# Optimization experiments

Hardware: AMD Instinct MI355X
Metric: run time of the kernel (lower is better)

Reference implementation:

```python
import jax, jax.numpy as jnp
import numpy as np

B, N, IN_DIM, HID = 64, 1024, 128, 32


def _xavier(key, shape):
    # xavier_uniform_ on torch Linear weight [out, in]; we store [in, out]
    fan_in, fan_out = shape[0], shape[1]
    limit = float(np.sqrt(6.0 / (fan_in + fan_out)))
    return jax.random.uniform(key, shape, jnp.float32, -limit, limit)


def setup_inputs() -> dict:
    key = jax.random.key(0)
    ks = jax.random.split(key, 8)
    x = jax.random.normal(ks[0], (B, N, IN_DIM), jnp.float32)
    adj = jax.random.uniform(ks[1], (B, N, N), jnp.float32)  # dense adjacency
    W1 = _xavier(ks[2], (IN_DIM, HID))
    W2 = _xavier(ks[3], (HID, HID))
    W3 = _xavier(ks[4], (HID, HID))
    W4 = _xavier(ks[5], (HID, HID))
    b1 = jnp.zeros((HID,), jnp.float32)
    b2 = jnp.zeros((HID,), jnp.float32)
    b3 = jnp.zeros((HID,), jnp.float32)
    b4 = jnp.zeros((HID,), jnp.float32)
    a1 = jnp.float32(0.25)  # PReLU default init
    a2 = jnp.float32(0.25)
    a3 = jnp.float32(0.25)
    a4 = jnp.float32(0.25)
    return {"x": x, "adj": adj, "W1": W1, "W2": W2, "W3": W3, "W4": W4,
            "b1": b1, "b2": b2, "b3": b3, "b4": b4,
            "a1": a1, "a2": a2, "a3": a3, "a4": a4}


def _gcn_layer(x, adj, W, b, a):
    h = jnp.einsum('bnf,fo->bno', x, W)      # linear, no bias
    h = jnp.matmul(adj, h) + b               # aggregation + bias
    return jnp.where(h >= 0, h, a * h)       # PReLU


def reference(x, adj, W1, W2, W3, W4, b1, b2, b3, b4, a1, a2, a3, a4):
    h1 = _gcn_layer(x, adj, W1, b1, a1)
    h2 = _gcn_layer(h1, adj, W2, b2, a2)
    h3 = _gcn_layer(h2, adj, W3, b3, a3)
    h4 = _gcn_layer(h3, adj, W4, b4, a4)
    # sum-pool nodes per layer, concat along feature dim -> [B, 4*HID]
    return jnp.concatenate([h1.sum(axis=1), h2.sum(axis=1),
                            h3.sum(axis=1), h4.sum(axis=1)], axis=1)
```

## Files before the change

### kernel.cpp

```cpp
#include <hip/hip_runtime.h>
#include <hip/hip_bf16.h>

#define B_   64
#define N_   1024
#define IND_ 128
#define HID_ 32

typedef __attribute__((ext_vector_type(8))) short short8;
typedef __attribute__((ext_vector_type(4))) float f32x4;
typedef unsigned short u16;

static __device__ __forceinline__ u16 f2bf(float f) {
    union { __hip_bfloat16 h; u16 s; } u;
    u.h = __float2bfloat16(f);
    return u.s;
}
static __device__ __forceinline__ short8 cvt8(f32x4 v0, f32x4 v1) {
    union { short8 s; __hip_bfloat162 h[4]; } u;
    u.h[0] = __float22bfloat162_rn(float2{v0[0], v0[1]});
    u.h[1] = __float22bfloat162_rn(float2{v0[2], v0[3]});
    u.h[2] = __float22bfloat162_rn(float2{v1[0], v1[1]});
    u.h[3] = __float22bfloat162_rn(float2{v1[2], v1[3]});
    return u.s;
}

__global__ __launch_bounds__(256) void convert_kernel(
    const float* __restrict__ adjf, u16* __restrict__ adjb)
{
    const size_t total = (size_t)B_ * N_ * N_ / 8;
    const size_t stride = (size_t)gridDim.x * 256;
    for (size_t i = (size_t)blockIdx.x * 256 + threadIdx.x; i < total; i += stride) {
        const f32x4* src = (const f32x4*)adjf + i * 2;
        f32x4 v0 = __builtin_nontemporal_load(src);
        f32x4 v1 = __builtin_nontemporal_load(src + 1);
        ((short8*)adjb)[i] = cvt8(v0, v1);
    }
}

template<int F>
__global__ __launch_bounds__(256) void linear_kernel(
    const float* __restrict__ in,
    const float* __restrict__ W,
    u16* __restrict__ outT)
{
    __shared__ float sW[F][HID_];
    const int tid = threadIdx.x;
    for (int e = tid; e < F * HID_; e += 256) sW[e / HID_][e % HID_] = W[e];
    __syncthreads();

    const int b = blockIdx.x >> 2;
    const int n = ((blockIdx.x & 3) << 8) + tid;
    const f32x4* row4 = (const f32x4*)(in + ((size_t)b * N_ + n) * F);

    float acc[HID_];
#pragma unroll
    for (int o = 0; o < HID_; ++o) acc[o] = 0.f;

#pragma unroll 4
    for (int f4 = 0; f4 < F / 4; ++f4) {
        f32x4 xv = row4[f4];
#pragma unroll
        for (int j = 0; j < 4; ++j) {
#pragma unroll
            for (int o = 0; o < HID_; ++o) acc[o] += xv[j] * sW[f4 * 4 + j][o];
        }
    }
    u16* op = outT + (size_t)b * HID_ * N_ + n;
#pragma unroll
    for (int o = 0; o < HID_; ++o) op[o * N_] = f2bf(acc[o]);
}

template<int MODE, int FUSE>
__global__ __launch_bounds__(256) void agg_kernel(
    const float* __restrict__ adjf,
    const u16*  __restrict__ adjb_in,
    const u16*  __restrict__ hlinT_in,
    u16*        __restrict__ hlinT_out,
    const float* __restrict__ Wnext,
    float*      __restrict__ h,
    float*      __restrict__ partial,
    const float* __restrict__ bias,
    const float* __restrict__ alpha_p)
{
    union Smem {
        u16 sB[HID_][512 + 8];
        struct { float h_s[64][33]; float sW2[HID_][HID_]; } ep;
    };
    __shared__ Smem sm;
    __shared__ float pool[4][HID_];

    const int tid = threadIdx.x;
    const int b = blockIdx.y;
    const int wid = tid >> 6, lane = tid & 63;
    const int r16 = lane & 15, g = lane >> 4;
    const int koff = g * 8;
    const int rowbase = blockIdx.x * 64 + wid * 16;
    const int row0 = rowbase + r16;
    const size_t adj_b = (size_t)b * N_ * N_;
    const u16* srcB = hlinT_in + (size_t)b * HID_ * N_;

    const u16*  pa = adjb_in ? adjb_in + adj_b + (size_t)row0 * N_ + koff : nullptr;
    const float* pf = adjf   ? adjf    + adj_b + (size_t)row0 * N_ + koff : nullptr;

    f32x4 acc[2] = {};

    for (int c = 0; c < 2; ++c) {
        if (c) __syncthreads();
        for (int i = tid; i < 2048; i += 256) {
            const int row = i >> 6;
            const int kv = (i & 63) << 3;
            *(short8*)&sm.sB[row][kv] =
                *(const short8*)(srcB + (size_t)row * N_ + (c << 9) + kv);
        }
        __syncthreads();

#pragma unroll 8
        for (int kk = 0; kk < 512; kk += 32) {
            const int k0 = (c << 9) + kk;
            short8 a0;
            if (MODE == 0) {
                a0 = *(const short8*)(pa + k0);
            } else {
                f32x4 v0 = __builtin_nontemporal_load((const f32x4*)(pf + k0));
                f32x4 v1 = __builtin_nontemporal_load((const f32x4*)(pf + k0) + 1);
                a0 = cvt8(v0, v1);
            }
            short8 b0 = *(const short8*)&sm.sB[r16][kk + koff];
            short8 b1 = *(const short8*)&sm.sB[16 + r16][kk + koff];
            acc[0] = __builtin_amdgcn_mfma_f32_16x16x32_bf16(a0, b0, acc[0], 0, 0, 0);
            acc[1] = __builtin_amdgcn_mfma_f32_16x16x32_bf16(a0, b1, acc[1], 0, 0, 0);
        }
    }

    const float alpha = *alpha_p;
    float v[2][4];
    float ps[2];
#pragma unroll
    for (int ct = 0; ct < 2; ++ct) {
        const float bv = bias[ct * 16 + r16];
        ps[ct] = 0.f;
#pragma unroll
        for (int r = 0; r < 4; ++r) {
            float x = acc[ct][r] + bv;
            x = (x >= 0.f) ? x : alpha * x;
            v[ct][r] = x;
            ps[ct] += x;
        }
    }

    __syncthreads();

#pragma unroll
    for (int ct = 0; ct < 2; ++ct) {
        const int col = ct * 16 + r16;
        float p = ps[ct];
        p += __shfl_xor(p, 16, 64);
        p += __shfl_xor(p, 32, 64);
        if (lane < 16) pool[wid][col] = p;
        if (FUSE) {
#pragma unroll
            for (int r = 0; r < 4; ++r)
                sm.ep.h_s[wid * 16 + g * 4 + r][col] = v[ct][r];
        }
        if (MODE == 2) {
#pragma unroll
            for (int r = 0; r < 4; ++r) {
                const int row = rowbase + g * 4 + r;
                h[((size_t)b * N_ + row) * HID_ + col] = v[ct][r];
            }
        }
    }
    if (FUSE) {
        for (int e = tid; e < HID_ * HID_; e += 256)
            ((float*)sm.ep.sW2)[e] = Wnext[e];
    }
    __syncthreads();

    if (tid < HID_) {
        float s = pool[0][tid] + pool[1][tid] + pool[2][tid] + pool[3][tid];
        partial[((size_t)b * 16 + blockIdx.x) * HID_ + tid] = s;
    }

    if (FUSE) {
        const int r_local = tid >> 2;
        const int obase = (tid & 3) * 8;
        float acc2[8];
#pragma unroll
        for (int o = 0; o < 8; ++o) acc2[o] = 0.f;
#pragma unroll 4
        for (int k = 0; k < HID_; ++k) {
            const float hv = sm.ep.h_s[r_local][k];
#pragma unroll
            for (int o = 0; o < 8; ++o) acc2[o] += hv * sm.ep.sW2[k][obase + o];
        }
        const int n = blockIdx.x * 64 + r_local;
        u16* op = hlinT_out + (size_t)b * HID_ * N_ + n;
#pragma unroll
        for (int o = 0; o < 8; ++o) op[(size_t)(obase + o) * N_] = f2bf(acc2[o]);
    }
}

__global__ __launch_bounds__(256) void finalize_kernel(
    const float* __restrict__ partial,
    float* __restrict__ out)
{
    const int i = blockIdx.x * 256 + threadIdx.x;
    if (i >= B_ * 4 * HID_) return;
    const int b = i >> 7;
    const int rem = i & 127;
    const int l = rem >> 5;
    const int o = rem & 31;
    const float* p = partial + (((size_t)l * B_ + b) * 16) * HID_ + o;
    float s = 0.f;
#pragma unroll
    for (int t = 0; t < 16; ++t) s += p[t * HID_];
    out[i] = s;
}

extern "C" void kernel_launch(void* const* d_in, const int* in_sizes, int n_in,
                              void* d_out, int out_size, void* d_ws, size_t ws_size,
                              hipStream_t stream) {
    const float* x   = (const float*)d_in[0];
    const float* adj = (const float*)d_in[1];
    const float* W[4]  = {(const float*)d_in[2], (const float*)d_in[3],
                          (const float*)d_in[4], (const float*)d_in[5]};
    const float* bi[4] = {(const float*)d_in[6], (const float*)d_in[7],
                          (const float*)d_in[8], (const float*)d_in[9]};
    const float* al[4] = {(const float*)d_in[10], (const float*)d_in[11],
                          (const float*)d_in[12], (const float*)d_in[13]};
    float* out = (float*)d_out;

    const size_t adjb_bytes = (size_t)B_ * N_ * N_ * 2;
    const size_t hlin_bytes = (size_t)B_ * HID_ * N_ * 2;
    const size_t h_bytes    = (size_t)B_ * N_ * HID_ * 4;
    const size_t part_bytes = (size_t)4 * B_ * 16 * HID_ * 4;
    const bool full = ws_size >= adjb_bytes + 2 * hlin_bytes + part_bytes;

    const dim3 ga(16, 64);
    const int part_stride = B_ * 16 * HID_;

    if (full) {
        char* p = (char*)d_ws;
        u16* adjb  = (u16*)p;  p += adjb_bytes;
        u16* hlinA = (u16*)p;  p += hlin_bytes;
        u16* hlinB = (u16*)p;  p += hlin_bytes;
        float* partial = (float*)p;

        convert_kernel<<<2048, 256, 0, stream>>>(adj, adjb);
        linear_kernel<IND_><<<256, 256, 0, stream>>>(x, W[0], hlinA);

        agg_kernel<0, 1><<<ga, 256, 0, stream>>>(nullptr, adjb, hlinA, hlinB,
                                                 W[1], nullptr,
                                                 partial + 0, bi[0], al[0]);
        agg_kernel<0, 1><<<ga, 256, 0, stream>>>(nullptr, adjb, hlinB, hlinA,
                                                 W[2], nullptr,
                                                 partial + (size_t)1 * part_stride,
                                                 bi[1], al[1]);
        agg_kernel<0, 1><<<ga, 256, 0, stream>>>(nullptr, adjb, hlinA, hlinB,
                                                 W[3], nullptr,
                                                 partial + (size_t)2 * part_stride,
                                                 bi[2], al[2]);
        agg_kernel<0, 0><<<ga, 256, 0, stream>>>(nullptr, adjb, hlinB, nullptr,
                                                 nullptr, nullptr,
                                                 partial + (size_t)3 * part_stride,
                                                 bi[3], al[3]);
    } else {
        char* p = (char*)d_ws;
        u16*   hlinT   = (u16*)p;  p += hlin_bytes;
        float* h       = (float*)p; p += h_bytes;
        float* partial = (float*)p;

        linear_kernel<IND_><<<256, 256, 0, stream>>>(x, W[0], hlinT);
        agg_kernel<2, 0><<<ga, 256, 0, stream>>>(adj, nullptr, hlinT, nullptr,
                                                 nullptr, h, partial + 0, bi[0], al[0]);
        for (int l = 1; l < 4; ++l) {
            linear_kernel<HID_><<<256, 256, 0, stream>>>(h, W[l], hlinT);
            agg_kernel<2, 0><<<ga, 256, 0, stream>>>(adj, nullptr, hlinT, nullptr,
                                                     nullptr, h,
                                                     partial + (size_t)l * part_stride,
                                                     bi[l], al[l]);
        }
    }
    finalize_kernel<<<32, 256, 0, stream>>>(
        (const float*)((char*)d_ws + (full ? adjb_bytes + 2 * hlin_bytes
                                           : hlin_bytes + h_bytes)), out);
}
```

Before: 213.7 us.

## Store bf16 adjacency in MFMA-fragment tiled layout for contiguous wave loads

The fp32-to-bf16 conversion now writes the adjacency in a tiled layout. Each wave's 16x32 A-fragment for one k-step occupies one contiguous 1 KB block. The aggregation kernels read these fragments with fully contiguous per-wave loads instead of 2 KB-strided row accesses, which should improve coalescing and cache-line use. The converter's stores are now ordered by tile rather than by linear position, and the layout ties the converter to the agg kernel's tiling.

```diff
diff --git a/kernel.cpp b/kernel.cpp
--- a/kernel.cpp
+++ b/kernel.cpp
@@ -24,16 +24,25 @@
     return u.s;
 }
 
-__global__ __launch_bounds__(256) void convert_kernel(
-    const float* __restrict__ adjf, u16* __restrict__ adjb)
+__global__ __launch_bounds__(256) void convert_tile_kernel(
+    const float* __restrict__ adjf, u16* __restrict__ adjT)
 {
-    const size_t total = (size_t)B_ * N_ * N_ / 8;
-    const size_t stride = (size_t)gridDim.x * 256;
-    for (size_t i = (size_t)blockIdx.x * 256 + threadIdx.x; i < total; i += stride) {
-        const f32x4* src = (const f32x4*)adjf + i * 2;
-        f32x4 v0 = __builtin_nontemporal_load(src);
-        f32x4 v1 = __builtin_nontemporal_load(src + 1);
-        ((short8*)adjb)[i] = cvt8(v0, v1);
+    const int wslot = blockIdx.x * 4 + (threadIdx.x >> 6);
+    const int lane = threadIdx.x & 63;
+    const int r = lane & 15, g = lane >> 4;
+    const int t0 = wslot * 16;
+    const int b  = t0 >> 11;
+    const int rt = (t0 >> 5) & 63;
+    const int k0base = (t0 & 31) * 32;
+
+    const float* src = adjf + ((size_t)b * N_ + rt * 16 + r) * N_ + k0base + g * 8;
+    u16* dst = adjT + (size_t)t0 * 512 + lane * 8;
+
+#pragma unroll 4
+    for (int j = 0; j < 16; ++j) {
+        f32x4 v0 = __builtin_nontemporal_load((const f32x4*)(src + j * 32));
+        f32x4 v1 = __builtin_nontemporal_load((const f32x4*)(src + j * 32) + 1);
+        *(short8*)(dst + (size_t)j * 512) = cvt8(v0, v1);
     }
 }
 
@@ -73,7 +82,7 @@
 template<int MODE, int FUSE>
 __global__ __launch_bounds__(256) void agg_kernel(
     const float* __restrict__ adjf,
-    const u16*  __restrict__ adjb_in,
+    const u16*  __restrict__ adjT,
     const u16*  __restrict__ hlinT_in,
     u16*        __restrict__ hlinT_out,
     const float* __restrict__ Wnext,
@@ -96,11 +105,14 @@
     const int koff = g * 8;
     const int rowbase = blockIdx.x * 64 + wid * 16;
     const int row0 = rowbase + r16;
-    const size_t adj_b = (size_t)b * N_ * N_;
     const u16* srcB = hlinT_in + (size_t)b * HID_ * N_;
 
-    const u16*  pa = adjb_in ? adjb_in + adj_b + (size_t)row0 * N_ + koff : nullptr;
-    const float* pf = adjf   ? adjf    + adj_b + (size_t)row0 * N_ + koff : nullptr;
+    const u16* pa = adjT
+        ? adjT + ((size_t)b * 2048 + (size_t)(blockIdx.x * 4 + wid) * 32) * 512 + lane * 8
+        : nullptr;
+    const float* pf = adjf
+        ? adjf + ((size_t)b * N_ + row0) * N_ + koff
+        : nullptr;
 
     f32x4 acc[2] = {};
 
@@ -116,11 +128,12 @@
 
 #pragma unroll 8
         for (int kk = 0; kk < 512; kk += 32) {
-            const int k0 = (c << 9) + kk;
             short8 a0;
             if (MODE == 0) {
-                a0 = *(const short8*)(pa + k0);
+                const int ki = c * 16 + (kk >> 5);
+                a0 = *(const short8*)(pa + (size_t)ki * 512);
             } else {
+                const int k0 = (c << 9) + kk;
                 f32x4 v0 = __builtin_nontemporal_load((const f32x4*)(pf + k0));
                 f32x4 v1 = __builtin_nontemporal_load((const f32x4*)(pf + k0) + 1);
                 a0 = cvt8(v0, v1);
@@ -241,26 +254,26 @@
 
     if (full) {
         char* p = (char*)d_ws;
-        u16* adjb  = (u16*)p;  p += adjb_bytes;
+        u16* adjT  = (u16*)p;  p += adjb_bytes;
         u16* hlinA = (u16*)p;  p += hlin_bytes;
         u16* hlinB = (u16*)p;  p += hlin_bytes;
         float* partial = (float*)p;
 
-        convert_kernel<<<2048, 256, 0, stream>>>(adj, adjb);
+        convert_tile_kernel<<<2048, 256, 0, stream>>>(adj, adjT);
         linear_kernel<IND_><<<256, 256, 0, stream>>>(x, W[0], hlinA);
 
-        agg_kernel<0, 1><<<ga, 256, 0, stream>>>(nullptr, adjb, hlinA, hlinB,
+        agg_kernel<0, 1><<<ga, 256, 0, stream>>>(nullptr, adjT, hlinA, hlinB,
                                                  W[1], nullptr,
                                                  partial + 0, bi[0], al[0]);
-        agg_kernel<0, 1><<<ga, 256, 0, stream>>>(nullptr, adjb, hlinB, hlinA,
+        agg_kernel<0, 1><<<ga, 256, 0, stream>>>(nullptr, adjT, hlinB, hlinA,
                                                  W[2], nullptr,
                                                  partial + (size_t)1 * part_stride,
                                                  bi[1], al[1]);
-        agg_kernel<0, 1><<<ga, 256, 0, stream>>>(nullptr, adjb, hlinA, hlinB,
+        agg_kernel<0, 1><<<ga, 256, 0, stream>>>(nullptr, adjT, hlinA, hlinB,
                                                  W[3], nullptr,
                                                  partial + (size_t)2 * part_stride,
                                                  bi[2], al[2]);
-        agg_kernel<0, 0><<<ga, 256, 0, stream>>>(nullptr, adjb, hlinB, nullptr,
+        agg_kernel<0, 0><<<ga, 256, 0, stream>>>(nullptr, adjT, hlinB, nullptr,
                                                  nullptr, nullptr,
                                                  partial + (size_t)3 * part_stride,
                                                  bi[3], al[3]);
```

Result: no change. 212.5 us (-0.6%).
